# Kernel optimization log

Measured on AMD Instinct MI355X. Metric: run time of the kernel, lower is better.

Reference implementation:

```python
import jax, jax.numpy as jnp
import numpy as np

NUM_TOKENS = 32000
BATCH = 8192
K = 10  # 'ten-hot'

def setup_inputs() -> dict:
    key = jax.random.key(0)
    x = jax.random.randint(key, (BATCH, K), 0, NUM_TOKENS, dtype=jnp.int64)
    return {"x": x}

def reference(x) -> jnp.ndarray:
    # Multi-hot encode: out[n, x[n, j]] = 1 for all j. Duplicate indices simply
    # re-write 1 (set, not add), matching the torch assignment semantics.
    B = x.shape[0]
    out = jnp.zeros((B, NUM_TOKENS), dtype=jnp.float32)
    rows = jnp.arange(B, dtype=x.dtype)[:, None]  # [B,1] broadcasts over K
    out = out.at[rows, x].set(1.0, mode="drop")
    return out
```

## Files before the change

### kernel.cpp

```cpp
#include <hip/hip_runtime.h>


#define NUM_TOKENS 32000
#define KHOT 10
#define BLOCK 256

typedef int i32x4 __attribute__((ext_vector_type(4)));

__global__ __launch_bounds__(BLOCK) void tenhot_scatter(
    const int* __restrict__ x, float* __restrict__ out, int total) {
    const int v = blockIdx.x * BLOCK + threadIdx.x;
    const int e0 = 4 * v;
    if (e0 >= total) return;
    const i32x4 q = *reinterpret_cast<const i32x4*>(x + e0);
    #pragma unroll
    for (int u = 0; u < 4; ++u) {
        const int e = e0 + u;
        if (e < total) {
            const int idx = q[u];
            if (idx >= 0 && idx < NUM_TOKENS) {
                const unsigned row = (unsigned)e / KHOT;
                out[(size_t)row * NUM_TOKENS + idx] = 1.0f;
            }
        }
    }
}

extern "C" void kernel_launch(void* const* d_in, const int* in_sizes, int n_in,
                              void* d_out, int out_size, void* d_ws, size_t ws_size,
                              hipStream_t stream) {
    const int* x = (const int*)d_in[0];
    float* out = (float*)d_out;
    const int total = in_sizes[0];
    hipMemsetAsync(d_out, 0, (size_t)out_size * sizeof(float), stream);
    const int nthreads = (total + 3) / 4;
    tenhot_scatter<<<(nthreads + BLOCK - 1) / BLOCK, BLOCK, 0, stream>>>(x, out, total);
}
```

Baseline: 188.8 us.

## Fuse zero-fill and scatter into one cooperative kernel with grid sync

```diff
diff --git a/kernel.cpp b/kernel.cpp
--- a/kernel.cpp
+++ b/kernel.cpp
@@ -1,28 +1,60 @@
 #include <hip/hip_runtime.h>
+#include <hip/hip_cooperative_groups.h>
+
+namespace cg = cooperative_groups;
 
 
 #define NUM_TOKENS 32000
 #define KHOT 10
 #define BLOCK 256
+#define GRID 256
+#define STRIDE (GRID * BLOCK)
+#define TOTAL_F4 65536000
+#define UNROLL 4
+#define ITERS (TOTAL_F4 / (STRIDE * UNROLL))
 
-typedef int i32x4 __attribute__((ext_vector_type(4)));
+typedef float f32x4 __attribute__((ext_vector_type(4)));
+typedef int   i32x4 __attribute__((ext_vector_type(4)));
 
-__global__ __launch_bounds__(BLOCK) void tenhot_scatter(
+__global__ __launch_bounds__(BLOCK) void tenhot_coop(
     const int* __restrict__ x, float* __restrict__ out, int total) {
-    const int v = blockIdx.x * BLOCK + threadIdx.x;
-    const int e0 = 4 * v;
-    if (e0 >= total) return;
-    const i32x4 q = *reinterpret_cast<const i32x4*>(x + e0);
+    const int t = threadIdx.x;
+    const int b = blockIdx.x;
+
+    const int per_blk = total / GRID;
+    size_t addr[4];
+    bool   val[4];
+    {
+        const int e0 = b * per_blk + 4 * t;
+        const bool live = (4 * t + 3) < per_blk;
+        i32x4 q = {0, 0, 0, 0};
+        if (live) q = *reinterpret_cast<const i32x4*>(x + e0);
+        #pragma unroll
+        for (int u = 0; u < 4; ++u) {
+            const int idx = q[u];
+            const int e = e0 + u;
+            val[u]  = live && (idx >= 0) && (idx < NUM_TOKENS);
+            addr[u] = (size_t)((unsigned)e / KHOT) * NUM_TOKENS + (size_t)(unsigned)idx;
+        }
+    }
+
+    f32x4* __restrict__ out4 = (f32x4*)out;
+    size_t i = (size_t)b * BLOCK + t;
+    const f32x4 z = {0.f, 0.f, 0.f, 0.f};
+    #pragma unroll 1
+    for (int k = 0; k < ITERS; ++k) {
+        out4[i]              = z;
+        out4[i + STRIDE]     = z;
+        out4[i + 2 * STRIDE] = z;
+        out4[i + 3 * STRIDE] = z;
+        i += (size_t)(UNROLL * STRIDE);
+    }
+
+    cg::this_grid().sync();
+
     #pragma unroll
     for (int u = 0; u < 4; ++u) {
-        const int e = e0 + u;
-        if (e < total) {
-            const int idx = q[u];
-            if (idx >= 0 && idx < NUM_TOKENS) {
-                const unsigned row = (unsigned)e / KHOT;
-                out[(size_t)row * NUM_TOKENS + idx] = 1.0f;
-            }
-        }
+        if (val[u]) out[addr[u]] = 1.0f;
     }
 }
 
@@ -31,8 +63,8 @@
                               hipStream_t stream) {
     const int* x = (const int*)d_in[0];
     float* out = (float*)d_out;
-    const int total = in_sizes[0];
-    hipMemsetAsync(d_out, 0, (size_t)out_size * sizeof(float), stream);
-    const int nthreads = (total + 3) / 4;
-    tenhot_scatter<<<(nthreads + BLOCK - 1) / BLOCK, BLOCK, 0, stream>>>(x, out, total);
+    int total = in_sizes[0];
+    void* args[] = {(void*)&x, (void*)&out, (void*)&total};
+    hipLaunchCooperativeKernel((void*)tenhot_coop, dim3(GRID), dim3(BLOCK),
+                               args, 0, stream);
 }
```

Result: slower. 241.2 us (+27.7%).
